# Performance work log

Hardware: AMD Instinct MI355X
Metric: run time of the kernel (lower is better)

The kernel has to match this reference:

```python
import jax, jax.numpy as jnp
import numpy as np

VOCAB, EMB, UNITS, B, T = 10000, 256, 1024, 64, 256


def gru_scan(x_seq, h0, W, U, b):
    """Keras GRU (reset_after=True) over time. x_seq: (T,B,E), h0: (B,H).
    W: (E,3H), U: (H,3H), b: (2,3H) [input bias, recurrent bias].
    Returns ys: (T,B,H), hT: (B,H)."""
    b_i, b_r = b[0], b[1]
    # precompute input projections for all timesteps in one big matmul
    xw = jnp.einsum('tbe,eh->tbh', x_seq, W) + b_i  # (T,B,3H)

    def step(h, xw_t):
        hu = h @ U + b_r                      # (B,3H)
        xz, xr, xh = jnp.split(xw_t, 3, axis=-1)
        hz, hr, hh = jnp.split(hu, 3, axis=-1)
        z = jax.nn.sigmoid(xz + hz)
        r = jax.nn.sigmoid(xr + hr)
        cand = jnp.tanh(xh + r * hh)          # reset applied AFTER recurrent matmul
        hn = z * h + (1.0 - z) * cand
        return hn, hn

    hT, ys = jax.lax.scan(step, h0, xw)
    return ys, hT


def setup_inputs() -> dict:
    key = jax.random.key(0)
    ks = jax.random.split(key, 8)
    x = jax.random.randint(ks[0], (B, T), 0, VOCAB)
    hidden = jnp.zeros((B, UNITS), dtype=jnp.float32)
    emb = jax.random.normal(ks[1], (VOCAB, EMB), dtype=jnp.float32) * 0.05
    sW = 1.0 / np.sqrt(EMB)
    sU = 1.0 / np.sqrt(UNITS)
    Wf = jax.random.normal(ks[2], (EMB, 3 * UNITS), dtype=jnp.float32) * sW
    Uf = jax.random.normal(ks[3], (UNITS, 3 * UNITS), dtype=jnp.float32) * sU
    bf = jnp.zeros((2, 3 * UNITS), dtype=jnp.float32)
    Wb = jax.random.normal(ks[4], (EMB, 3 * UNITS), dtype=jnp.float32) * sW
    Ub = jax.random.normal(ks[5], (UNITS, 3 * UNITS), dtype=jnp.float32) * sU
    bb = jnp.zeros((2, 3 * UNITS), dtype=jnp.float32)
    return {"x": x, "hidden": hidden, "emb": emb,
            "Wf": Wf, "Uf": Uf, "bf": bf, "Wb": Wb, "Ub": Ub, "bb": bb}


def reference(x, hidden, emb, Wf, Uf, bf, Wb, Ub, bb):
    e = emb[x]                      # (B,T,E) embedding lookup
    xs = jnp.transpose(e, (1, 0, 2))  # (T,B,E) time-major for scan
    yf, hf = gru_scan(xs, hidden, Wf, Uf, bf)
    yb_rev, hb = gru_scan(xs[::-1], hidden, Wb, Ub, bb)
    yb = yb_rev[::-1]               # align backward outputs with original time
    concat = jnp.transpose(jnp.concatenate([yf, yb], axis=-1), (1, 0, 2))  # (B,T,2H)
    return concat, hf, hb
```

## Files before the change

kernel.cpp:

```cpp
#include <hip/hip_runtime.h>
#include <stdint.h>

#define TT 256
#define BBATCH 64
#define EE 256
#define HHID 1024

typedef __attribute__((ext_vector_type(8))) short bf16x8;
typedef __attribute__((ext_vector_type(4))) float f32x4;
typedef __attribute__((ext_vector_type(4))) unsigned short u16x4;
typedef __attribute__((ext_vector_type(4))) unsigned int u32x4;

#define WS_CNT   0
#define WS_H     4096
#define WS_EMBB  (4096 + 4*131072)
#define WS_WT    (WS_EMBB + 10000*256*2)
#define WS_XW    (WS_WT + (size_t)2*3072*256*2)
#define WS_TOTAL (WS_XW + (size_t)2*16384*3072*2)

__device__ __forceinline__ unsigned short f2bf(float f) {
  union { float f; unsigned u; } v; v.f = f;
  unsigned r = v.u + 0x7fffu + ((v.u >> 16) & 1u);
  return (unsigned short)(r >> 16);
}
__device__ __forceinline__ float bf2f(unsigned short b) {
  union { unsigned u; float f; } v; v.u = ((unsigned)b) << 16;
  return v.f;
}
__device__ __forceinline__ bf16x8 as_bf(u32x4 v) {
  union { u32x4 u; bf16x8 h; } c; c.u = v; return c.h;
}

__device__ __forceinline__ u32x4 ld_bypass16(const unsigned short* p) {
  u32x4 d;
  asm volatile("global_load_dwordx4 %0, %1, off sc0 sc1" : "=v"(d) : "v"(p));
  return d;
}
__device__ __forceinline__ unsigned ld_bypass_u16(const unsigned short* p) {
  unsigned d;
  asm volatile("global_load_ushort %0, %1, off sc0 sc1" : "=v"(d) : "v"(p));
  return d;
}
__device__ __forceinline__ void st_bypass_u16(unsigned short* p, unsigned v) {
  asm volatile("global_store_short %0, %1, off sc0 sc1" :: "v"(p), "v"(v));
}
__device__ __forceinline__ void drain_vm() {
  asm volatile("s_waitcnt vmcnt(0)" ::: "memory");
}
__device__ __forceinline__ void wait_cnt(unsigned* cnt, unsigned tgt) {
  while (__hip_atomic_load(cnt, __ATOMIC_RELAXED, __HIP_MEMORY_SCOPE_AGENT) < tgt)
    __builtin_amdgcn_s_sleep(1);
}

#define G_ISSUE(buf, base) do { \
  _Pragma("unroll") for (int kk = 0; kk < 8; ++kk) \
    buf[kk] = ld_bypass16(hrow + ((base) + kk) * 32); } while (0)

#define G_WAIT8(buf) asm volatile("s_waitcnt vmcnt(8)" \
  : "+v"(buf[0]), "+v"(buf[1]), "+v"(buf[2]), "+v"(buf[3]), \
    "+v"(buf[4]), "+v"(buf[5]), "+v"(buf[6]), "+v"(buf[7]))
#define G_WAIT8H(buf) asm volatile("s_waitcnt vmcnt(8)" \
  : "+v"(buf[0]), "+v"(buf[1]), "+v"(buf[2]), "+v"(buf[3]), \
    "+v"(buf[4]), "+v"(buf[5]), "+v"(buf[6]), "+v"(buf[7]), \
    "+v"(hv0), "+v"(hv1), "+v"(hv2), "+v"(hv3))
#define G_WAIT0(buf) asm volatile("s_waitcnt vmcnt(0)" \
  : "+v"(buf[0]), "+v"(buf[1]), "+v"(buf[2]), "+v"(buf[3]), \
    "+v"(buf[4]), "+v"(buf[5]), "+v"(buf[6]), "+v"(buf[7]))

#define MFMA_G(buf, base) do { \
  _Pragma("unroll") for (int kk = 0; kk < 8; ++kk) { \
    bf16x8 a = as_bf(buf[kk]); \
    az = __builtin_amdgcn_mfma_f32_16x16x32_bf16(a, Ufr[0][(base) + kk], az, 0, 0, 0); \
    ar = __builtin_amdgcn_mfma_f32_16x16x32_bf16(a, Ufr[1][(base) + kk], ar, 0, 0, 0); \
    ah = __builtin_amdgcn_mfma_f32_16x16x32_bf16(a, Ufr[2][(base) + kk], ah, 0, 0, 0); \
  } } while (0)

__global__ void cvt_emb_k(const float* __restrict__ emb, unsigned short* __restrict__ embb) {
  int i = (blockIdx.x * 256 + threadIdx.x) * 4;
  if (i >= 10000 * 256) return;
  f32x4 v = *(const f32x4*)(emb + i);
  u16x4 o;
  o[0] = f2bf(v[0]); o[1] = f2bf(v[1]); o[2] = f2bf(v[2]); o[3] = f2bf(v[3]);
  *(u16x4*)(embb + i) = o;
}

__global__ void wt_k(const float* __restrict__ Wf, const float* __restrict__ Wb,
                     unsigned short* __restrict__ wt) {
  int n = blockIdx.x * 256 + threadIdx.x;
  int dir = blockIdx.z;
  const float* W = dir ? Wb : Wf;
  unsigned short* o = wt + ((size_t)dir * 3072 + n) * 256;
  int k0 = blockIdx.y * 16;
#pragma unroll
  for (int k = 0; k < 16; ++k)
    o[k0 + k] = f2bf(W[(size_t)(k0 + k) * 3072 + n]);
}

__global__ __launch_bounds__(256) void xw_gemm_k(
    const int* __restrict__ x, const unsigned short* __restrict__ embb,
    const unsigned short* __restrict__ wt,
    const float* __restrict__ bfp, const float* __restrict__ bbp,
    unsigned short* __restrict__ xw) {
  int tid = threadIdx.x, lane = tid & 63, wave = tid >> 6;
  int wm = wave & 1, wn = wave >> 1;
  int dir = blockIdx.z;
  int m0 = blockIdx.x * 128 + wm * 64;
  int n0 = blockIdx.y * 128 + wn * 64;
  int l15 = lane & 15, lhi = (lane >> 4) << 3;

  const unsigned short* wtd = wt + (size_t)dir * 3072 * 256;

  int tok[4];
#pragma unroll
  for (int mt = 0; mt < 4; ++mt) {
    int gm = m0 + mt * 16 + l15;
    tok[mt] = x[(gm & 63) * TT + (gm >> 6)];
  }

  f32x4 zero4 = {0.f, 0.f, 0.f, 0.f};
  f32x4 acc[4][4];
#pragma unroll
  for (int mt = 0; mt < 4; ++mt)
#pragma unroll
    for (int nt = 0; nt < 4; ++nt) acc[mt][nt] = zero4;

#pragma unroll
  for (int kc = 0; kc < 8; ++kc) {
    bf16x8 a[4], b[4];
#pragma unroll
    for (int mt = 0; mt < 4; ++mt)
      a[mt] = *(const bf16x8*)(embb + (size_t)tok[mt] * 256 + kc * 32 + lhi);
#pragma unroll
    for (int nt = 0; nt < 4; ++nt)
      b[nt] = *(const bf16x8*)(wtd + (size_t)(n0 + nt * 16 + l15) * 256 + kc * 32 + lhi);
#pragma unroll
    for (int mt = 0; mt < 4; ++mt)
#pragma unroll
      for (int nt = 0; nt < 4; ++nt)
        acc[mt][nt] = __builtin_amdgcn_mfma_f32_16x16x32_bf16(a[mt], b[nt], acc[mt][nt], 0, 0, 0);
  }

  const float* bia = dir ? bbp : bfp;
  float bn[4];
#pragma unroll
  for (int nt = 0; nt < 4; ++nt) bn[nt] = bia[n0 + nt * 16 + l15];

  unsigned short* xwd = xw + (size_t)dir * 16384 * 3072;
#pragma unroll
  for (int mt = 0; mt < 4; ++mt) {
#pragma unroll
    for (int rr = 0; rr < 4; ++rr) {
      int gm = m0 + mt * 16 + ((lane >> 4) << 2) + rr;
#pragma unroll
      for (int nt = 0; nt < 4; ++nt) {
        unsigned short v = f2bf(acc[mt][nt][rr] + bn[nt]);
        __builtin_nontemporal_store(v, xwd + (size_t)gm * 3072 + n0 + nt * 16 + l15);
      }
    }
  }
}

__global__ __launch_bounds__(256, 1) void gru_k(
    const float* __restrict__ Uf, const float* __restrict__ Ub,
    const float* __restrict__ bfp, const float* __restrict__ bbp,
    const float* __restrict__ h0,
    float* __restrict__ out, unsigned char* __restrict__ ws) {
  int tid = threadIdx.x, lane = tid & 63, wave = tid >> 6;
  int dir = blockIdx.x & 1, cg = blockIdx.x >> 1;
  int c0 = cg * 16;
  int l15 = lane & 15, lq = lane >> 4;

  unsigned* cnt = (unsigned*)(ws + (size_t)dir * 256);
  unsigned short* hb0 = (unsigned short*)(ws + WS_H + (size_t)dir * 262144);
  unsigned short* hb1 = (unsigned short*)(ws + WS_H + (size_t)dir * 262144 + 131072);
  const unsigned short* xwd = (const unsigned short*)(ws + WS_XW) + (size_t)dir * 16384 * 3072;

  const float* U = dir ? Ub : Uf;
  const float* bia = dir ? bbp : bfp;

  __shared__ unsigned short uts[16][1032];
  bf16x8 Ufr[3][32];
  for (int g = 0; g < 3; ++g) {
    __syncthreads();
    int p = tid & 3, kk0 = tid >> 2;
#pragma unroll 1
    for (int i = 0; i < 16; ++i) {
      int k = i * 64 + kk0;
      f32x4 v = *(const f32x4*)(U + (size_t)k * 3072 + g * 1024 + c0 + p * 4);
#pragma unroll
      for (int j = 0; j < 4; ++j) uts[p * 4 + j][k] = f2bf(v[j]);
    }
    __syncthreads();
#pragma unroll
    for (int ks = 0; ks < 32; ++ks)
      Ufr[g][ks] = *(const bf16x8*)&uts[l15][ks * 32 + lq * 8];
  }
  float br[3];
#pragma unroll
  for (int g = 0; g < 3; ++g) br[g] = bia[3072 + g * 1024 + c0 + l15];

  for (int i = tid; i < 1024; i += 256) {
    int b = i >> 4, c = c0 + (i & 15);
    st_bypass_u16(&hb0[b * 1024 + c], (unsigned)f2bf(h0[b * 1024 + c]));
  }
  drain_vm();
  __syncthreads();
  if (tid == 0)
    __hip_atomic_fetch_add(cnt, 1u, __ATOMIC_RELAXED, __HIP_MEMORY_SCOPE_AGENT);

  int cidx = c0 + l15;
  int rb = wave * 16 + lq * 4;
  const int hrow_off = (wave * 16 + l15) * 1024 + lq * 8;

  unsigned short xv[3][4];
  {
    int t = dir ? 255 : 0;
#pragma unroll
    for (int g = 0; g < 3; ++g)
#pragma unroll
      for (int rr = 0; rr < 4; ++rr)
        xv[g][rr] = xwd[(size_t)(t * 64 + rb + rr) * 3072 + g * 1024 + cidx];
  }

  if (tid == 0) wait_cnt(cnt, 64u);
  __syncthreads();

  float* hT = out + 33554432 + (dir ? 65536 : 0);

#pragma unroll 1
  for (int s = 0; s < 256; ++s) {
    unsigned short* hpb = (s & 1) ? hb1 : hb0;
    unsigned short* hn = (s & 1) ? hb0 : hb1;
    int t = dir ? (255 - s) : s;

    unsigned hv0 = ld_bypass_u16(hpb + (rb + 0) * 1024 + cidx);
    unsigned hv1 = ld_bypass_u16(hpb + (rb + 1) * 1024 + cidx);
    unsigned hv2 = ld_bypass_u16(hpb + (rb + 2) * 1024 + cidx);
    unsigned hv3 = ld_bypass_u16(hpb + (rb + 3) * 1024 + cidx);

    const unsigned short* hrow = hpb + hrow_off;
    f32x4 az = {0.f, 0.f, 0.f, 0.f}, ar = az, ah = az;
    u32x4 ga[8], gb[8];
    G_ISSUE(ga, 0);
    G_ISSUE(gb, 8);
    G_WAIT8H(ga);
    MFMA_G(ga, 0);
    G_ISSUE(ga, 16);
    G_WAIT8(gb);
    MFMA_G(gb, 8);
    G_ISSUE(gb, 24);
    G_WAIT8(ga);
    MFMA_G(ga, 16);
    G_WAIT0(gb);
    MFMA_G(gb, 24);

    unsigned hv[4] = {hv0, hv1, hv2, hv3};
#pragma unroll
    for (int rr = 0; rr < 4; ++rr) {
      float hz = az[rr] + br[0];
      float hr = ar[rr] + br[1];
      float hh = ah[rr] + br[2];
      float xz = bf2f((unsigned short)xv[0][rr]);
      float xr = bf2f((unsigned short)xv[1][rr]);
      float xh = bf2f((unsigned short)xv[2][rr]);
      float z = 1.0f / (1.0f + __expf(-(xz + hz)));
      float r = 1.0f / (1.0f + __expf(-(xr + hr)));
      float cand = 1.0f - 2.0f / (1.0f + __expf(2.0f * (xh + r * hh)));
      float hnew = z * bf2f((unsigned short)hv[rr]) + (1.0f - z) * cand;
      int b = rb + rr;
      st_bypass_u16(&hn[b * 1024 + cidx], (unsigned)f2bf(hnew));
      __builtin_nontemporal_store(hnew, out + ((size_t)b * 256 + t) * 2048 + dir * 1024 + cidx);
      if (s == 255) hT[b * 1024 + cidx] = hnew;
    }

    if (s == 255) break;

    drain_vm();
    __syncthreads();
    if (tid == 0)
      __hip_atomic_fetch_add(cnt, 1u, __ATOMIC_RELAXED, __HIP_MEMORY_SCOPE_AGENT);

    {
      int t2 = dir ? (254 - s) : (s + 1);
#pragma unroll
      for (int g = 0; g < 3; ++g)
#pragma unroll
        for (int rr = 0; rr < 4; ++rr)
          xv[g][rr] = xwd[(size_t)(t2 * 64 + rb + rr) * 3072 + g * 1024 + cidx];
    }

    if (tid == 0) wait_cnt(cnt, 64u * (unsigned)(s + 2));
    __syncthreads();
  }
}

__global__ void diag_k(float* out, float v) { out[0] = v; }

extern "C" void kernel_launch(void* const* d_in, const int* in_sizes, int n_in,
                              void* d_out, int out_size, void* d_ws, size_t ws_size,
                              hipStream_t stream) {
  (void)in_sizes; (void)n_in; (void)out_size;
  const int*   x      = (const int*)d_in[0];
  const float* hidden = (const float*)d_in[1];
  const float* emb    = (const float*)d_in[2];
  const float* Wf     = (const float*)d_in[3];
  const float* Uf     = (const float*)d_in[4];
  const float* bf_    = (const float*)d_in[5];
  const float* Wb     = (const float*)d_in[6];
  const float* Ub     = (const float*)d_in[7];
  const float* bb_    = (const float*)d_in[8];
  float* out = (float*)d_out;
  unsigned char* ws = (unsigned char*)d_ws;

  if (ws_size < WS_TOTAL) {
    diag_k<<<1, 1, 0, stream>>>(out, (float)ws_size);
    return;
  }

  hipMemsetAsync(ws, 0, 4096, stream);
  cvt_emb_k<<<2500, 256, 0, stream>>>(emb, (unsigned short*)(ws + WS_EMBB));
  wt_k<<<dim3(12, 16, 2), 256, 0, stream>>>(Wf, Wb, (unsigned short*)(ws + WS_WT));
  xw_gemm_k<<<dim3(128, 24, 2), 256, 0, stream>>>(
      x, (const unsigned short*)(ws + WS_EMBB), (const unsigned short*)(ws + WS_WT),
      bf_, bb_, (unsigned short*)(ws + WS_XW));
  gru_k<<<128, 256, 0, stream>>>(Uf, Ub, bf_, bb_, hidden, out, ws);
}
```

Baseline: 2.201 ms.

## Use a rotating hidden-state ring buffer with cached loads and periodic acquire fences

Replaces the two ping-pong hidden-state buffers with a 32-slot ring buffer per direction. Because each step reads a fresh address range, the per-step reads of h can use normal cached loads instead of cache-bypassing sc0/sc1 loads. Stale cache lines are cleared by an agent-scope acquire fence every 16 steps. The aim is to cut the global-memory latency on the serial recurrence path. The risk is coherence: correctness depends on no stale lines surviving between ring reuses and on a fence issued only by thread 0 being enough across the XCD caches.

Result: no change. 2.189 ms (-0.5%).

```diff
diff --git a/kernel.cpp b/kernel.cpp
--- a/kernel.cpp
+++ b/kernel.cpp
@@ -12,8 +12,9 @@
 typedef __attribute__((ext_vector_type(4))) unsigned int u32x4;
 
 #define WS_CNT   0
-#define WS_H     4096
-#define WS_EMBB  (4096 + 4*131072)
+#define HROT_N   32
+#define WS_HROT  4096
+#define WS_EMBB  (WS_HROT + 2*HROT_N*131072)
 #define WS_WT    (WS_EMBB + 10000*256*2)
 #define WS_XW    (WS_WT + (size_t)2*3072*256*2)
 #define WS_TOTAL (WS_XW + (size_t)2*16384*3072*2)
@@ -31,18 +32,18 @@
   union { u32x4 u; bf16x8 h; } c; c.u = v; return c.h;
 }
 
-__device__ __forceinline__ u32x4 ld_bypass16(const unsigned short* p) {
-  u32x4 d;
-  asm volatile("global_load_dwordx4 %0, %1, off sc0 sc1" : "=v"(d) : "v"(p));
-  return d;
-}
-__device__ __forceinline__ unsigned ld_bypass_u16(const unsigned short* p) {
-  unsigned d;
-  asm volatile("global_load_ushort %0, %1, off sc0 sc1" : "=v"(d) : "v"(p));
-  return d;
-}
 __device__ __forceinline__ void st_bypass_u16(unsigned short* p, unsigned v) {
   asm volatile("global_store_short %0, %1, off sc0 sc1" :: "v"(p), "v"(v));
+}
+__device__ __forceinline__ u32x4 ld_c16(const unsigned short* p) {
+  u32x4 d;
+  asm volatile("global_load_dwordx4 %0, %1, off" : "=v"(d) : "v"(p));
+  return d;
+}
+__device__ __forceinline__ unsigned ld_c_u16(const unsigned short* p) {
+  unsigned d;
+  asm volatile("global_load_ushort %0, %1, off" : "=v"(d) : "v"(p));
+  return d;
 }
 __device__ __forceinline__ void drain_vm() {
   asm volatile("s_waitcnt vmcnt(0)" ::: "memory");
@@ -54,7 +55,7 @@
 
 #define G_ISSUE(buf, base) do { \
   _Pragma("unroll") for (int kk = 0; kk < 8; ++kk) \
-    buf[kk] = ld_bypass16(hrow + ((base) + kk) * 32); } while (0)
+    buf[kk] = ld_c16(hrow + ((base) + kk) * 32); } while (0)
 
 #define G_WAIT8(buf) asm volatile("s_waitcnt vmcnt(8)" \
   : "+v"(buf[0]), "+v"(buf[1]), "+v"(buf[2]), "+v"(buf[3]), \
@@ -171,8 +172,7 @@
   int l15 = lane & 15, lq = lane >> 4;
 
   unsigned* cnt = (unsigned*)(ws + (size_t)dir * 256);
-  unsigned short* hb0 = (unsigned short*)(ws + WS_H + (size_t)dir * 262144);
-  unsigned short* hb1 = (unsigned short*)(ws + WS_H + (size_t)dir * 262144 + 131072);
+  unsigned short* hrot = (unsigned short*)(ws + WS_HROT) + (size_t)dir * HROT_N * 65536;
   const unsigned short* xwd = (const unsigned short*)(ws + WS_XW) + (size_t)dir * 16384 * 3072;
 
   const float* U = dir ? Ub : Uf;
@@ -201,7 +201,7 @@
 
   for (int i = tid; i < 1024; i += 256) {
     int b = i >> 4, c = c0 + (i & 15);
-    st_bypass_u16(&hb0[b * 1024 + c], (unsigned)f2bf(h0[b * 1024 + c]));
+    st_bypass_u16(&hrot[b * 1024 + c], (unsigned)f2bf(h0[b * 1024 + c]));
   }
   drain_vm();
   __syncthreads();
@@ -229,14 +229,14 @@
 
 #pragma unroll 1
   for (int s = 0; s < 256; ++s) {
-    unsigned short* hpb = (s & 1) ? hb1 : hb0;
-    unsigned short* hn = (s & 1) ? hb0 : hb1;
+    const unsigned short* hpb = hrot + (size_t)(s & (HROT_N - 1)) * 65536;
+    unsigned short* hn = hrot + (size_t)((s + 1) & (HROT_N - 1)) * 65536;
     int t = dir ? (255 - s) : s;
 
-    unsigned hv0 = ld_bypass_u16(hpb + (rb + 0) * 1024 + cidx);
-    unsigned hv1 = ld_bypass_u16(hpb + (rb + 1) * 1024 + cidx);
-    unsigned hv2 = ld_bypass_u16(hpb + (rb + 2) * 1024 + cidx);
-    unsigned hv3 = ld_bypass_u16(hpb + (rb + 3) * 1024 + cidx);
+    unsigned hv0 = ld_c_u16(hpb + (rb + 0) * 1024 + cidx);
+    unsigned hv1 = ld_c_u16(hpb + (rb + 1) * 1024 + cidx);
+    unsigned hv2 = ld_c_u16(hpb + (rb + 2) * 1024 + cidx);
+    unsigned hv3 = ld_c_u16(hpb + (rb + 3) * 1024 + cidx);
 
     const unsigned short* hrow = hpb + hrow_off;
     f32x4 az = {0.f, 0.f, 0.f, 0.f}, ar = az, ah = az;
@@ -289,7 +289,11 @@
           xv[g][rr] = xwd[(size_t)(t2 * 64 + rb + rr) * 3072 + g * 1024 + cidx];
     }
 
-    if (tid == 0) wait_cnt(cnt, 64u * (unsigned)(s + 2));
+    if (tid == 0) {
+      wait_cnt(cnt, 64u * (unsigned)(s + 2));
+      if (((s + 1) & 15) == 0)
+        __builtin_amdgcn_fence(__ATOMIC_ACQUIRE, "agent");
+    }
     __syncthreads();
   }
 }
```
